# Kernel optimization log

Measured on AMD Instinct MI355X. Metric: run time of the kernel, lower is better.

## Reference

```python
import jax, jax.numpy as jnp
import numpy as np

NUM, K = 5, 3
IN_DIM, D_OUT = 512, 512
N_U, BATCH, GATED_IN = 64, 8192, 576
NB = NUM + K + 1  # 9 basis channels (num+k splines + 1 SiLU base)
TERM_SIZES = (4, 8)
TERM_MULTS = (32768, 16384)  # 4*32768 + 8*16384 = 262144 = D_OUT*IN_DIM
WDIM = 128


def extend_grid(grid, k):
    # grid: (S, num+1) -> (S, num+1+2k), appending k knots each side with uniform spacing h
    h = (grid[:, -1:] - grid[:, :1]) / (grid.shape[1] - 1)
    left = grid[:, :1] + h * jnp.arange(-k, 0, dtype=grid.dtype)
    right = grid[:, -1:] + h * jnp.arange(1, k + 1, dtype=grid.dtype)
    return jnp.concatenate([left, grid, right], axis=1)


def B_batch(x, grid, k):
    # Cox-de-Boor recursion. x: (S, B), grid: (S, G) extended. Returns (S, G-k-1, B).
    xg = x[:, None, :]
    g = grid[:, :, None]
    v = ((xg >= g[:, :-1]) & (xg < g[:, 1:])).astype(x.dtype)
    for p in range(1, k + 1):
        v = (xg - g[:, :-(p + 1)]) / (g[:, p:-1] - g[:, :-(p + 1)]) * v[:, :-1] \
          + (g[:, p + 1:] - xg) / (g[:, p + 1:] - g[:, 1:-p]) * v[:, 1:]
    return v


def lazy_P(terms, mults, perm, w):
    # emlp-style lazy equivariant projector: permute rows, apply small block
    # projectors with multiplicities, un-permute. w: (R, C).
    invperm = jnp.argsort(perm)
    wp = w[perm]
    outs, off = [], 0
    for P, m in zip(terms, mults):
        s = P.shape[0]
        blk = wp[off:off + m * s].reshape(m, s, -1)
        outs.append(jnp.einsum('ij,mjc->mic', P, blk).reshape(m * s, -1))
        off += m * s
    return jnp.concatenate(outs, axis=0)[invperm]


def setup_inputs() -> dict:
    key = jax.random.key(0)
    ks = jax.random.split(key, 12)
    x = jax.random.normal(ks[0], (BATCH, GATED_IN), dtype=jnp.float32)
    grid = jnp.tile(jnp.linspace(-1.0, 1.0, NUM + 1, dtype=jnp.float32)[None, :], (N_U, 1))
    linear_weight = 0.05 * jax.random.normal(ks[1], (D_OUT, NB * IN_DIM), dtype=jnp.float32)
    linear_bias = 0.05 * jax.random.normal(ks[2], (D_OUT,), dtype=jnp.float32)
    P_term_a = 0.3 * jax.random.normal(ks[3], (TERM_SIZES[0], TERM_SIZES[0]), dtype=jnp.float32)
    P_term_b = 0.3 * jax.random.normal(ks[4], (TERM_SIZES[1], TERM_SIZES[1]), dtype=jnp.float32)
    Pb = (1.0 / np.sqrt(D_OUT)) * jax.random.normal(ks[5], (D_OUT, D_OUT), dtype=jnp.float32)
    bi_basis = 0.01 * jax.random.normal(ks[6], (WDIM, D_OUT, D_OUT), dtype=jnp.float32)
    bi_w = jax.random.normal(ks[7], (WDIM,), dtype=jnp.float32)
    u = jnp.sort(jax.random.randint(ks[8], (N_U,), 0, GATED_IN))
    indices = jax.random.randint(ks[9], (IN_DIM,), 0, N_U)
    perm = jax.random.permutation(ks[10], D_OUT * IN_DIM)
    return {"x": x, "grid": grid, "linear_weight": linear_weight, "linear_bias": linear_bias,
            "P_term_a": P_term_a, "P_term_b": P_term_b, "Pb": Pb,
            "bi_basis": bi_basis, "bi_w": bi_w, "u": u, "indices": indices, "perm": perm}


def reference(x, grid, linear_weight, linear_bias, P_term_a, P_term_b, Pb, bi_basis, bi_w, u, indices, perm):
    batch = x.shape[0]
    # gather gate scalars and build spline + base activations
    gs = x[:, u].T                                   # (S, B)
    eg = extend_grid(grid, K)                        # (S, num+1+2k)
    sp = B_batch(gs, eg, K)                          # (S, num+k, B)
    sp = jnp.transpose(sp, (2, 1, 0))                # (B, num+k, S)
    sb = jax.nn.silu(gs).T[:, None, :]               # (B, 1, S)
    g = jnp.concatenate([sp, sb], axis=1)            # (B, NB, S)
    g = g[:, :, indices]                             # (B, NB, in_dim) gather via inverse indices
    acts = (g * x[:, None, :IN_DIM]).reshape(batch, -1)  # (B, NB*in_dim)
    # equivariant weight projection
    w_r = linear_weight.reshape(D_OUT, NB, IN_DIM).transpose(0, 2, 1).reshape(D_OUT * IN_DIM, NB)
    W_r = lazy_P([P_term_a, P_term_b], TERM_MULTS, perm, w_r)
    W = W_r.reshape(D_OUT, IN_DIM, NB).transpose(0, 2, 1).reshape(D_OUT, NB * IN_DIM)
    b = Pb @ linear_bias
    out = acts @ W.T + b                             # (B, D_OUT)
    # bilinear equivariant mix
    bi_W = jnp.einsum('w,wij->ij', bi_w, bi_basis)   # (D_OUT, D_OUT)
    out = 0.1 * (out @ bi_W.T) + out
    return out
```

## Files before the change

kernel.cpp:

```cpp
#include <hip/hip_runtime.h>

#define DI __device__ __forceinline__

typedef __attribute__((ext_vector_type(8))) short short8;
typedef __attribute__((ext_vector_type(4))) float f32x4;

DI ushort f2bf(float f) {
  union { float f; unsigned u; } v; v.f = f;
  unsigned r = v.u + 0x7fffu + ((v.u >> 16) & 1u);
  return (ushort)(r >> 16);
}

DI void gload_lds16(const void* g, void* l) {
  __builtin_amdgcn_global_load_lds((const __attribute__((address_space(1))) void*)g,
                                   (__attribute__((address_space(3))) void*)l, 16, 0, 0);
}


__global__ __launch_bounds__(256) void k_biW(const float2* __restrict__ bb,
                                             const float* __restrict__ bw,
                                             float2* __restrict__ Mf32,
                                             uint* __restrict__ Mbf16) {
  __shared__ float w[128];
  int tid = threadIdx.x;
  if (tid < 128) w[tid] = bw[tid];
  __syncthreads();
  int t = blockIdx.x * 256 + tid;
  const float2* p = bb + t;
  float ax = 0.f, ay = 0.f;
#pragma unroll 8
  for (int k = 0; k < 128; ++k) {
    float2 v = p[(size_t)k * 131072];
    float s = w[k];
    ax += s * v.x; ay += s * v.y;
  }
  int i = t >> 8, j0 = (t & 255) * 2;
  float2 r;
  r.x = 0.1f * ax + (i == j0 + 0 ? 1.f : 0.f);
  r.y = 0.1f * ay + (i == j0 + 1 ? 1.f : 0.f);
  Mf32[t] = r;
  Mbf16[t] = (uint)f2bf(r.x) | ((uint)f2bf(r.y) << 16);
}

__global__ __launch_bounds__(256) void k_matvec(const float* __restrict__ A,
                                                const float* __restrict__ v,
                                                float* __restrict__ y) {
  int o = blockIdx.x * 4 + (threadIdx.x >> 6);
  int lane = threadIdx.x & 63;
  float acc = 0.f;
  for (int k = lane; k < 512; k += 64) acc += A[o * 512 + k] * v[k];
#pragma unroll
  for (int s = 32; s; s >>= 1) acc += __shfl_down(acc, s, 64);
  if (lane == 0) y[o] = acc;
}

__global__ __launch_bounds__(256) void k_lazyP(const float* __restrict__ LW,
                                               const float* __restrict__ Pa,
                                               const float* __restrict__ Pb8,
                                               const int* __restrict__ perm,
                                               ushort* __restrict__ Wt) {
  int q = blockIdx.x * 256 + threadIdx.x;
  int lane = threadIdx.x & 63;
  int r = perm[q];
  int o = r >> 9, ic = r & 511;
  int a_own = o * 4608 + ic;
  if (q < 131072) {
    int ii = lane & 3, g = lane & ~3;
    float pp[4];
#pragma unroll
    for (int j = 0; j < 4; ++j) pp[j] = Pa[ii * 4 + j];
#pragma unroll
    for (int c = 0; c < 9; ++c) {
      float v = LW[a_own + c * 512];
      float acc = 0.f;
#pragma unroll
      for (int j = 0; j < 4; ++j) acc += pp[j] * __shfl(v, g + j, 64);
      Wt[(size_t)(c * 512 + ic) * 512 + o] = f2bf(acc);
    }
  } else {
    int ii = lane & 7, g = lane & ~7;
    float pp[8];
#pragma unroll
    for (int j = 0; j < 8; ++j) pp[j] = Pb8[ii * 8 + j];
#pragma unroll
    for (int c = 0; c < 9; ++c) {
      float v = LW[a_own + c * 512];
      float acc = 0.f;
#pragma unroll
      for (int j = 0; j < 8; ++j) acc += pp[j] * __shfl(v, g + j, 64);
      Wt[(size_t)(c * 512 + ic) * 512 + o] = f2bf(acc);
    }
  }
}

__global__ __launch_bounds__(256) void k_acts(const float* __restrict__ x,
                                              const float* __restrict__ grid,
                                              const int* __restrict__ u,
                                              const int* __restrict__ indices,
                                              ushort* __restrict__ acts) {
  __shared__ float basis[8][64][9];
  __shared__ int sidx[512];
  int tid = threadIdx.x;
  int b0 = blockIdx.x * 8;
  for (int i = tid; i < 512; i += 256) sidx[i] = indices[i];
#pragma unroll
  for (int e0 = 0; e0 < 2; ++e0) {
    int e = e0 * 256 + tid;
    int row = e >> 6, j = e & 63;
    float gs = x[(size_t)(b0 + row) * 576 + u[j]];
    float g0 = grid[j * 6], g5 = grid[j * 6 + 5];
    float h = (g5 - g0) * 0.2f;
    float lo = g0 - 3.f * h;
    float tt = (gs - lo) / h;
#pragma unroll
    for (int n = 0; n < 8; ++n) basis[row][j][n] = 0.f;
    float fc = floorf(tt);
    int c = (int)fc;
    if (c >= 0 && c <= 10) {
      float t = tt - fc;
      float t2 = t * t, t3 = t2 * t;
      float om = 1.f - t;
      float w0 = t3 * (1.f / 6.f);
      float w1 = (1.f + 3.f * t + 3.f * t2 - 3.f * t3) * (1.f / 6.f);
      float w2 = (4.f - 6.f * t2 + 3.f * t3) * (1.f / 6.f);
      float w3 = om * om * om * (1.f / 6.f);
      if (c <= 7) basis[row][j][c] = w0;
      if (c >= 1 && c <= 8) basis[row][j][c - 1] = w1;
      if (c >= 2 && c <= 9) basis[row][j][c - 2] = w2;
      if (c >= 3) basis[row][j][c - 3] = w3;
    }
    basis[row][j][8] = gs / (1.f + __expf(-gs));
  }
  __syncthreads();
#pragma unroll
  for (int rep = 0; rep < 2; ++rep) {
    int e = rep * 256 + tid;
    int row = e >> 6, i0 = (e & 63) * 8;
    size_t xb = (size_t)(b0 + row) * 576;
    float4 xa = *(const float4*)&x[xb + i0];
    float4 xc = *(const float4*)&x[xb + i0 + 4];
    int4 ja = *(const int4*)&sidx[i0];
    int4 jb = *(const int4*)&sidx[i0 + 4];
    size_t ab = (size_t)(b0 + row) * 4608 + i0;
#pragma unroll
    for (int n = 0; n < 9; ++n) {
      short8 hv;
      hv[0] = (short)f2bf(basis[row][ja.x][n] * xa.x);
      hv[1] = (short)f2bf(basis[row][ja.y][n] * xa.y);
      hv[2] = (short)f2bf(basis[row][ja.z][n] * xa.z);
      hv[3] = (short)f2bf(basis[row][ja.w][n] * xa.w);
      hv[4] = (short)f2bf(basis[row][jb.x][n] * xc.x);
      hv[5] = (short)f2bf(basis[row][jb.y][n] * xc.y);
      hv[6] = (short)f2bf(basis[row][jb.z][n] * xc.z);
      hv[7] = (short)f2bf(basis[row][jb.w][n] * xc.w);
      *(short8*)(&acts[ab + (size_t)n * 512]) = hv;
    }
  }
}

template <int BM, int BN>
__global__ __launch_bounds__(256) void gemm_bt(const ushort* __restrict__ A,
                                               const ushort* __restrict__ B,
                                               ushort* __restrict__ Cout,
                                               int N, int Kd) {
  constexpr int BK = 64;
  constexpr int FM = BM / 32;
  constexpr int FN = BN / 32;
  __shared__ __align__(16) ushort Al[2][BM * BK];
  __shared__ __align__(16) ushort Bl[2][BN * BK];
  int tid = threadIdx.x, lane = tid & 63, wid = tid >> 6;
  int wm = wid >> 1, wn = wid & 1;
  int tiles_n = N / BN;
  int per_xcd = gridDim.x >> 3;
  int flat = (blockIdx.x & 7) * per_xcd + (blockIdx.x >> 3);
  int bm = flat / tiles_n, bn = flat % tiles_n;
  long m0 = (long)bm * BM;
  long n0 = (long)bn * BN;
  int swc = ((tid & 7) ^ ((tid >> 3) & 7)) * 8;
  const ushort* agp = A + (m0 + (tid >> 3)) * (long)Kd + swc;
  const ushort* bgp = B + (n0 + (tid >> 3)) * (long)Kd + swc;

#define STAGE64(buf, k0)                                                      \
  do {                                                                        \
    _Pragma("unroll")                                                         \
    for (int it = 0; it < BM / 32; ++it)                                      \
      gload_lds16(agp + (it * 32) * (long)Kd + (k0), &Al[buf][(it * 256 + tid) * 8]); \
    _Pragma("unroll")                                                         \
    for (int it = 0; it < BN / 32; ++it)                                      \
      gload_lds16(bgp + (it * 32) * (long)Kd + (k0), &Bl[buf][(it * 256 + tid) * 8]); \
  } while (0)

  f32x4 acc[FM][FN] = {};
  int swz = (lane & 7) << 3;
  int nt = Kd / BK;
  STAGE64(0, 0);
  __syncthreads();
  for (int t = 0; t < nt; ++t) {
    int cur = t & 1;
    if (t + 1 < nt) STAGE64(cur ^ 1, (t + 1) * BK);
#pragma unroll
    for (int ks = 0; ks < 2; ++ks) {
      int kidx = (ks * 32 + (lane >> 4) * 8) ^ swz;
      short8 a[FM], b[FN];
#pragma unroll
      for (int f = 0; f < FM; ++f)
        a[f] = *(const short8*)&Al[cur][(wm * (FM * 16) + f * 16 + (lane & 15)) * BK + kidx];
#pragma unroll
      for (int f = 0; f < FN; ++f)
        b[f] = *(const short8*)&Bl[cur][(wn * (FN * 16) + f * 16 + (lane & 15)) * BK + kidx];
#pragma unroll
      for (int i = 0; i < FM; ++i)
#pragma unroll
        for (int j = 0; j < FN; ++j)
          acc[i][j] = __builtin_amdgcn_mfma_f32_16x16x32_bf16(a[i], b[j], acc[i][j], 0, 0, 0);
    }
    __syncthreads();
  }
#undef STAGE64
#pragma unroll
  for (int i = 0; i < FM; ++i)
#pragma unroll
    for (int j = 0; j < FN; ++j) {
      int row_b = wm * (FM * 16) + i * 16 + ((lane >> 4) * 4);
      long col = n0 + wn * (FN * 16) + j * 16 + (lane & 15);
#pragma unroll
      for (int r = 0; r < 4; ++r)
        Cout[(m0 + row_b + r) * N + col] = f2bf(acc[i][j][r]);
    }
}

__global__ __launch_bounds__(256, 4) void gemm_sk(const ushort* __restrict__ A,
                                                  const ushort* __restrict__ B,
                                                  const float* __restrict__ b2,
                                                  float* __restrict__ P0,
                                                  float* __restrict__ P1,
                                                  float* __restrict__ P2,
                                                  float* __restrict__ P3) {
  constexpr int BM = 128, BN = 128, BK = 32, FM = 4, FN = 4;
  const int Kd = 4608, N = 512;
  __shared__ __align__(16) ushort Al[2][BM * BK];
  __shared__ __align__(16) ushort Bl[2][BN * BK];
  int tid = threadIdx.x, lane = tid & 63, wid = tid >> 6;
  int wm = wid >> 1, wn = wid & 1;
  int flat = (blockIdx.x & 7) * 128 + (blockIdx.x >> 3);
  int bm = flat >> 4, kb = (flat >> 2) & 3, bn = flat & 3;
  long m0 = (long)bm * BM, n0 = (long)bn * BN;
  int kbase = kb * 1152;
  float* Pout = kb == 0 ? P0 : kb == 1 ? P1 : kb == 2 ? P2 : P3;

  int r0 = tid >> 2, c0 = tid & 3;
  int swc = (c0 ^ ((r0 >> 1) & 3)) * 8;
  const ushort* agp = A + (m0 + r0) * (long)Kd + kbase + swc;
  const ushort* bgp = B + (n0 + r0) * (long)Kd + kbase + swc;

#define STAGE32(buf, k0)                                                      \
  do {                                                                        \
    _Pragma("unroll")                                                         \
    for (int it = 0; it < 2; ++it)                                            \
      gload_lds16(agp + (it * 64) * (long)Kd + (k0), &Al[buf][it * 2048 + tid * 8]); \
    _Pragma("unroll")                                                         \
    for (int it = 0; it < 2; ++it)                                            \
      gload_lds16(bgp + (it * 64) * (long)Kd + (k0), &Bl[buf][it * 2048 + tid * 8]); \
  } while (0)

  f32x4 acc[FM][FN] = {};
  const int nt = 1152 / BK;
  int e0 = lane >> 4;
  STAGE32(0, 0);
  __syncthreads();
  for (int t = 0; t < nt; ++t) {
    int cur = t & 1;
    if (t + 1 < nt) STAGE32(cur ^ 1, (t + 1) * BK);
    short8 a[FM], b[FN];
#pragma unroll
    for (int f = 0; f < FM; ++f) {
      int fr = wm * 64 + f * 16 + (lane & 15);
      a[f] = *(const short8*)&Al[cur][fr * BK + ((e0 ^ ((fr >> 1) & 3)) * 8)];
    }
#pragma unroll
    for (int f = 0; f < FN; ++f) {
      int fr = wn * 64 + f * 16 + (lane & 15);
      b[f] = *(const short8*)&Bl[cur][fr * BK + ((e0 ^ ((fr >> 1) & 3)) * 8)];
    }
#pragma unroll
    for (int i = 0; i < FM; ++i)
#pragma unroll
      for (int j = 0; j < FN; ++j)
        acc[i][j] = __builtin_amdgcn_mfma_f32_16x16x32_bf16(a[i], b[j], acc[i][j], 0, 0, 0);
    __syncthreads();
  }
#undef STAGE32
#pragma unroll
  for (int i = 0; i < FM; ++i)
#pragma unroll
    for (int j = 0; j < FN; ++j) {
      int row_b = wm * 64 + i * 16 + ((lane >> 4) * 4);
      long col = n0 + wn * 64 + j * 16 + (lane & 15);
      float bv = (kb == 0) ? b2[col] : 0.f;
#pragma unroll
      for (int r = 0; r < 4; ++r)
        Pout[(m0 + row_b + r) * N + col] = acc[i][j][r] + bv;
    }
}

__global__ __launch_bounds__(256) void k_reduce(float4* __restrict__ P0,
                                                const float4* __restrict__ P1,
                                                const float4* __restrict__ P2,
                                                const float4* __restrict__ P3) {
  int t = blockIdx.x * 256 + threadIdx.x;
#pragma unroll
  for (int rep = 0; rep < 2; ++rep) {
    int e = rep * 524288 + t;
    float4 a = P0[e], b = P1[e], c = P2[e], d = P3[e];
    a.x += b.x + c.x + d.x;
    a.y += b.y + c.y + d.y;
    a.z += b.z + c.z + d.z;
    a.w += b.w + c.w + d.w;
    P0[e] = a;
  }
}

extern "C" void kernel_launch(void* const* d_in, const int* in_sizes, int n_in,
                              void* d_out, int out_size, void* d_ws, size_t ws_size,
                              hipStream_t stream) {
  const float* x        = (const float*)d_in[0];
  const float* grid     = (const float*)d_in[1];
  const float* LW       = (const float*)d_in[2];
  const float* lb       = (const float*)d_in[3];
  const float* Pa       = (const float*)d_in[4];
  const float* Pb8      = (const float*)d_in[5];
  const float* Pbm      = (const float*)d_in[6];
  const float* bi_basis = (const float*)d_in[7];
  const float* bi_w     = (const float*)d_in[8];
  const int*   u        = (const int*)d_in[9];
  const int*   indices  = (const int*)d_in[10];
  const int*   perm     = (const int*)d_in[11];
  float* out = (float*)d_out;
  char* ws = (char*)d_ws;

  float*  Mf32  = (float*)(ws + 0);
  ushort* Mbf16 = (ushort*)(ws + 1048576);
  float*  tvec  = (float*)(ws + 1572864);
  float*  b2    = (float*)(ws + 1576960);
  ushort* Wt    = (ushort*)(ws + 2097152);
  ushort* W2    = (ushort*)(ws + 6815744);
  ushort* acts  = (ushort*)(ws + 11534336);
  float*  P1    = (float*)(ws + 87031808);
  float*  P2    = (float*)(ws + 103809024);
  float*  P3    = (float*)(ws + 120586240);

  k_biW<<<512, 256, 0, stream>>>((const float2*)bi_basis, bi_w, (float2*)Mf32, (uint*)Mbf16);
  k_matvec<<<128, 256, 0, stream>>>(Pbm, lb, tvec);
  k_matvec<<<128, 256, 0, stream>>>(Mf32, tvec, b2);
  k_lazyP<<<1024, 256, 0, stream>>>(LW, Pa, Pb8, perm, Wt);
  gemm_bt<128, 128><<<(512 / 128) * (4608 / 128), 256, 0, stream>>>(
      Mbf16, Wt, W2, 4608, 512);
  k_acts<<<1024, 256, 0, stream>>>(x, grid, u, indices, acts);
  gemm_sk<<<1024, 256, 0, stream>>>(acts, W2, b2, out, P1, P2, P3);
  k_reduce<<<2048, 256, 0, stream>>>((float4*)out, (const float4*)P1,
                                     (const float4*)P2, (const float4*)P3);
}
```

Measured before the change: 183.4 us.

## Use two-wave 128x64-per-wave tiling in split-K GEMM and retune tiles

The split-K GEMM now runs 128 threads (two waves) per block instead of 256. Each wave computes a 128x64 output strip with 8x4 MFMA fragments, so every loaded B fragment is reused across twice as many A rows and LDS read traffic per MFMA drops. Each thread now issues four global-to-LDS loads per operand per stage. The projection GEMM tile changes from 128x128 to 64x128, and the bi-basis reduction loop is unrolled further. The trade-off is fewer resident waves to hide latency and a doubled accumulator register footprint, which may lower occupancy.

New measurement: 186.6 us. Within noise of the previous version (+1.8%).

```diff
diff --git a/kernel.cpp b/kernel.cpp
--- a/kernel.cpp
+++ b/kernel.cpp
@@ -28,7 +28,7 @@
   int t = blockIdx.x * 256 + tid;
   const float2* p = bb + t;
   float ax = 0.f, ay = 0.f;
-#pragma unroll 8
+#pragma unroll 16
   for (int k = 0; k < 128; ++k) {
     float2 v = p[(size_t)k * 131072];
     float s = w[k];
@@ -229,59 +229,56 @@
     }
 }
 
-__global__ __launch_bounds__(256, 4) void gemm_sk(const ushort* __restrict__ A,
+__global__ __launch_bounds__(128, 2) void gemm_sk(const ushort* __restrict__ A,
                                                   const ushort* __restrict__ B,
                                                   const float* __restrict__ b2,
                                                   float* __restrict__ P0,
                                                   float* __restrict__ P1,
                                                   float* __restrict__ P2,
                                                   float* __restrict__ P3) {
-  constexpr int BM = 128, BN = 128, BK = 32, FM = 4, FN = 4;
+  constexpr int BK = 32, FM = 8, FN = 4;
   const int Kd = 4608, N = 512;
-  __shared__ __align__(16) ushort Al[2][BM * BK];
-  __shared__ __align__(16) ushort Bl[2][BN * BK];
-  int tid = threadIdx.x, lane = tid & 63, wid = tid >> 6;
-  int wm = wid >> 1, wn = wid & 1;
+  __shared__ __align__(16) ushort Al[2][128 * BK];
+  __shared__ __align__(16) ushort Bl[2][128 * BK];
+  int tid = threadIdx.x;
+  int lane = tid & 63, wn = tid >> 6;
   int flat = (blockIdx.x & 7) * 128 + (blockIdx.x >> 3);
   int bm = flat >> 4, kb = (flat >> 2) & 3, bn = flat & 3;
-  long m0 = (long)bm * BM, n0 = (long)bn * BN;
+  long m0 = (long)bm * 128, n0 = (long)bn * 128;
   int kbase = kb * 1152;
   float* Pout = kb == 0 ? P0 : kb == 1 ? P1 : kb == 2 ? P2 : P3;
 
-  int r0 = tid >> 2, c0 = tid & 3;
-  int swc = (c0 ^ ((r0 >> 1) & 3)) * 8;
-  const ushort* agp = A + (m0 + r0) * (long)Kd + kbase + swc;
-  const ushort* bgp = B + (n0 + r0) * (long)Kd + kbase + swc;
-
-#define STAGE32(buf, k0)                                                      \
+  int swc = ((tid & 3) ^ ((tid >> 3) & 3)) * 8;
+  const ushort* agp = A + (m0 + (tid >> 2)) * (long)Kd + kbase + swc;
+  const ushort* bgp = B + (n0 + (tid >> 2)) * (long)Kd + kbase + swc;
+
+#define STAGE(buf, k0)                                                        \
   do {                                                                        \
     _Pragma("unroll")                                                         \
-    for (int it = 0; it < 2; ++it)                                            \
-      gload_lds16(agp + (it * 64) * (long)Kd + (k0), &Al[buf][it * 2048 + tid * 8]); \
+    for (int it = 0; it < 4; ++it)                                            \
+      gload_lds16(agp + (it * 32) * (long)Kd + (k0), &Al[buf][(it * 128 + tid) * 8]); \
     _Pragma("unroll")                                                         \
-    for (int it = 0; it < 2; ++it)                                            \
-      gload_lds16(bgp + (it * 64) * (long)Kd + (k0), &Bl[buf][it * 2048 + tid * 8]); \
+    for (int it = 0; it < 4; ++it)                                            \
+      gload_lds16(bgp + (it * 32) * (long)Kd + (k0), &Bl[buf][(it * 128 + tid) * 8]); \
   } while (0)
 
   f32x4 acc[FM][FN] = {};
   const int nt = 1152 / BK;
-  int e0 = lane >> 4;
-  STAGE32(0, 0);
+  int ch = lane >> 4;
+  int cs = (lane >> 1) & 3;
+  int kidx = ((ch ^ cs) * 8);
+  STAGE(0, 0);
   __syncthreads();
   for (int t = 0; t < nt; ++t) {
     int cur = t & 1;
-    if (t + 1 < nt) STAGE32(cur ^ 1, (t + 1) * BK);
+    if (t + 1 < nt) STAGE(cur ^ 1, (t + 1) * BK);
     short8 a[FM], b[FN];
 #pragma unroll
-    for (int f = 0; f < FM; ++f) {
-      int fr = wm * 64 + f * 16 + (lane & 15);
-      a[f] = *(const short8*)&Al[cur][fr * BK + ((e0 ^ ((fr >> 1) & 3)) * 8)];
-    }
-#pragma unroll
-    for (int f = 0; f < FN; ++f) {
-      int fr = wn * 64 + f * 16 + (lane & 15);
-      b[f] = *(const short8*)&Bl[cur][fr * BK + ((e0 ^ ((fr >> 1) & 3)) * 8)];
-    }
+    for (int f = 0; f < FM; ++f)
+      a[f] = *(const short8*)&Al[cur][(f * 16 + (lane & 15)) * BK + kidx];
+#pragma unroll
+    for (int f = 0; f < FN; ++f)
+      b[f] = *(const short8*)&Bl[cur][(wn * 64 + f * 16 + (lane & 15)) * BK + kidx];
 #pragma unroll
     for (int i = 0; i < FM; ++i)
 #pragma unroll
@@ -289,12 +286,12 @@
         acc[i][j] = __builtin_amdgcn_mfma_f32_16x16x32_bf16(a[i], b[j], acc[i][j], 0, 0, 0);
     __syncthreads();
   }
-#undef STAGE32
+#undef STAGE
 #pragma unroll
   for (int i = 0; i < FM; ++i)
 #pragma unroll
     for (int j = 0; j < FN; ++j) {
-      int row_b = wm * 64 + i * 16 + ((lane >> 4) * 4);
+      int row_b = i * 16 + ((lane >> 4) * 4);
       long col = n0 + wn * 64 + j * 16 + (lane & 15);
       float bv = (kb == 0) ? b2[col] : 0.f;
 #pragma unroll
@@ -353,10 +350,10 @@
   k_matvec<<<128, 256, 0, stream>>>(Pbm, lb, tvec);
   k_matvec<<<128, 256, 0, stream>>>(Mf32, tvec, b2);
   k_lazyP<<<1024, 256, 0, stream>>>(LW, Pa, Pb8, perm, Wt);
-  gemm_bt<128, 128><<<(512 / 128) * (4608 / 128), 256, 0, stream>>>(
+  gemm_bt<64, 128><<<(512 / 64) * (4608 / 128), 256, 0, stream>>>(
       Mbf16, Wt, W2, 4608, 512);
   k_acts<<<1024, 256, 0, stream>>>(x, grid, u, indices, acts);
-  gemm_sk<<<1024, 256, 0, stream>>>(acts, W2, b2, out, P1, P2, P3);
+  gemm_sk<<<1024, 128, 0, stream>>>(acts, W2, b2, out, P1, P2, P3);
   k_reduce<<<2048, 256, 0, stream>>>((float4*)out, (const float4*)P1,
                                      (const float4*)P2, (const float4*)P3);
 }
```
